# Kernel optimization log

Hardware: AMD Instinct MI355X
Metric: run time of the kernel (lower is better)

Reference implementation:

```python
import jax, jax.numpy as jnp
import numpy as np


def setup_inputs() -> dict:
    key = jax.random.key(0)
    B, D = 8192, 4096
    ks = jax.random.split(key, 6)
    s = 1.0 / np.sqrt(D)  # nn.init.uniform_(-1/sqrt(D), 1/sqrt(D))
    return {
        "u": jax.random.normal(ks[0], (B, D), dtype=jnp.float32),
        "w1": jax.random.uniform(ks[1], (D,), jnp.float32, -s, s),
        "w2": jax.random.uniform(ks[2], (D,), jnp.float32, -s, s),
        "w3": jax.random.uniform(ks[3], (D,), jnp.float32, -s, s),
        "bias1": jnp.ones((1,), jnp.float32),
        "bias2": jnp.ones((1,), jnp.float32),
        # nn.Linear(D, 1): kaiming-uniform-ish init approximated with same bound
        "delta_w": jax.random.uniform(ks[4], (1, D), jnp.float32, -s, s),
        "delta_b": jax.random.uniform(ks[5], (1,), jnp.float32, -s, s),
    }


def reference(u, w1, w2, w3, bias1, bias2, delta_w, delta_b):
    # select = softplus(delta(u) + bias1), shape [B]
    select = jax.nn.softplus(u @ delta_w.T + delta_b + bias1)[:, 0]
    # einsum('bi,b->b', M, x) == (sum_i M[b,i]) * x[b], so the recurrence
    # collapses to scalar-per-batch coefficients:
    a = select * (u @ w1)   # sum_i Abar[b,i] = select[b] * sum_i w1[i]*u[b,i]
    b = u @ w2              # sum_i Bbar[b,i]
    c = u @ w3              # sum_i Cbar[b,i]
    Dc = bias2[0]
    ut = u.T                # [T, B], time-major for scan; T == input_dim
    x0 = b * ut[0]          # xi at step 0; y[:,0] = x0 (no C/D term in original)

    def step(x, ui):
        xn = a * x + b * ui
        return xn, c * xn + Dc * ui

    _, ys = jax.lax.scan(step, x0, ut[1:])  # ys: [T-1, B]
    y = jnp.concatenate([x0[None, :], ys], axis=0).T  # [B, T]
    return y
```

## Files before the change

kernel.cpp:

```cpp
#include <hip/hip_runtime.h>
#include <math.h>


#define DDIM 4096
#define NCH  16

__device__ __forceinline__ float clf(float v) {
    int b   = __float_as_int(v);
    int mag = b & 0x7fffffff;
    if (mag >= 0x7F7A0000)
        v = __int_as_float((b & 0x80000000) | 0x7F7A0000);
    return v;
}

__device__ __forceinline__ float softplus_ref(float z) {
    return (z > 0.0f) ? (z + log1pf(expf(-z))) : log1pf(expf(z));
}

__global__ __launch_bounds__(256) void ssm_kernel(
    const float* __restrict__ u,
    const float* __restrict__ w1,
    const float* __restrict__ w2,
    const float* __restrict__ w3,
    const float* __restrict__ bias1,
    const float* __restrict__ bias2,
    const float* __restrict__ dw,
    const float* __restrict__ db,
    float* __restrict__ y)
{
    const int wid  = threadIdx.x >> 6;
    const int lane = threadIdx.x & 63;
    const int row  = (blockIdx.x << 2) + wid;

    const float* __restrict__ urow = u + (size_t)row * DDIM;
    float* __restrict__ yrow       = y + (size_t)row * DDIM;

    float4 uv[NCH];
    float s0 = 0.f, s1 = 0.f, s2 = 0.f, s3 = 0.f;
#pragma unroll
    for (int c = 0; c < NCH; ++c) {
        const int idx = c * 256 + lane * 4;
        uv[c] = *reinterpret_cast<const float4*>(urow + idx);
        const float4 dv = *reinterpret_cast<const float4*>(dw + idx);
        const float4 a1 = *reinterpret_cast<const float4*>(w1 + idx);
        const float4 a2 = *reinterpret_cast<const float4*>(w2 + idx);
        const float4 a3 = *reinterpret_cast<const float4*>(w3 + idx);
        s0 += uv[c].x * dv.x + uv[c].y * dv.y + uv[c].z * dv.z + uv[c].w * dv.w;
        s1 += uv[c].x * a1.x + uv[c].y * a1.y + uv[c].z * a1.z + uv[c].w * a1.w;
        s2 += uv[c].x * a2.x + uv[c].y * a2.y + uv[c].z * a2.z + uv[c].w * a2.w;
        s3 += uv[c].x * a3.x + uv[c].y * a3.y + uv[c].z * a3.z + uv[c].w * a3.w;
    }
#pragma unroll
    for (int d = 1; d < 64; d <<= 1) {
        s0 += __shfl_xor(s0, d, 64);
        s1 += __shfl_xor(s1, d, 64);
        s2 += __shfl_xor(s2, d, 64);
        s3 += __shfl_xor(s3, d, 64);
    }

    const float sel = softplus_ref(s0 + db[0] + bias1[0]);
    const float a   = clf(sel * s1);
    const float bb  = s2;
    const float cc  = s3;
    const float Dc  = bias2[0];

    const float a2p  = clf(a * a);
    const float r1   = clf(a2p * a2p);
    const float r2   = clf(r1 * r1);
    const float r4   = clf(r2 * r2);
    const float r8   = clf(r4 * r4);
    const float r16  = clf(r8 * r8);
    const float r32  = clf(r16 * r16);
    const float a256 = clf(r32 * r32);
    float P = 1.0f;
    if (lane & 1)  P = clf(P * r1);
    if (lane & 2)  P = clf(P * r2);
    if (lane & 4)  P = clf(P * r4);
    if (lane & 8)  P = clf(P * r8);
    if (lane & 16) P = clf(P * r16);
    if (lane & 32) P = clf(P * r32);

    float Bv[NCH];
#pragma unroll
    for (int c = 0; c < NCH; ++c) {
        float B = bb * uv[c].x;
        B = fmaf(a, B, bb * uv[c].y);
        B = fmaf(a, B, bb * uv[c].z);
        B = fmaf(a, B, bb * uv[c].w);
        Bv[c] = clf(B);
    }

#pragma unroll
    for (int c = 0; c < NCH; ++c) {
        float B = Bv[c];
        float t;
        t = __shfl_up(B, 1,  64); if (lane >= 1)  B = clf(fmaf(r1,  t, B));
        t = __shfl_up(B, 2,  64); if (lane >= 2)  B = clf(fmaf(r2,  t, B));
        t = __shfl_up(B, 4,  64); if (lane >= 4)  B = clf(fmaf(r4,  t, B));
        t = __shfl_up(B, 8,  64); if (lane >= 8)  B = clf(fmaf(r8,  t, B));
        t = __shfl_up(B, 16, 64); if (lane >= 16) B = clf(fmaf(r16, t, B));
        t = __shfl_up(B, 32, 64); if (lane >= 32) B = clf(fmaf(r32, t, B));
        Bv[c] = B;
    }

    float cr = 0.0f;
#pragma unroll
    for (int c = 0; c < NCH; ++c) {
        const int idx = c * 256 + lane * 4;
        const float T = __shfl(Bv[c], 63, 64);
        float Cprev   = __shfl_up(Bv[c], 1, 64);
        if (lane == 0) Cprev = 0.0f;

        const float xs = clf(fmaf(P, cr, Cprev));
        const float x0 = clf(fmaf(a, xs, bb * uv[c].x));
        const float x1 = clf(fmaf(a, x0, bb * uv[c].y));
        const float x2 = clf(fmaf(a, x1, bb * uv[c].z));
        const float x3 = clf(fmaf(a, x2, bb * uv[c].w));

        float4 yv;
        yv.x = clf(fmaf(cc, x0, Dc * uv[c].x));
        yv.y = clf(fmaf(cc, x1, Dc * uv[c].y));
        yv.z = clf(fmaf(cc, x2, Dc * uv[c].z));
        yv.w = clf(fmaf(cc, x3, Dc * uv[c].w));
        if (c == 0 && lane == 0) yv.x = x0;
        *reinterpret_cast<float4*>(yrow + idx) = yv;

        cr = clf(fmaf(a256, cr, T));
    }
}

extern "C" void kernel_launch(void* const* d_in, const int* in_sizes, int n_in,
                              void* d_out, int out_size, void* d_ws, size_t ws_size,
                              hipStream_t stream) {
    const float* u     = (const float*)d_in[0];
    const float* w1    = (const float*)d_in[1];
    const float* w2    = (const float*)d_in[2];
    const float* w3    = (const float*)d_in[3];
    const float* bias1 = (const float*)d_in[4];
    const float* bias2 = (const float*)d_in[5];
    const float* dw    = (const float*)d_in[6];
    const float* db    = (const float*)d_in[7];
    float* y = (float*)d_out;

    const int B = in_sizes[0] / DDIM;
    dim3 grid(B / 4), block(256);
    hipLaunchKernelGGL(ssm_kernel, grid, block, 0, stream,
                       u, w1, w2, w3, bias1, bias2, dw, db, y);
}
```

Measured before the change: 251.3 us.

## Split each row across four waves with LDS reduction and cross-wave scan carry

Each 256-thread block now handles one row instead of four, with each wave covering a quarter of the row. Dot-product partials are combined through shared memory, and the carry between waves is built from per-wave totals using a1024 powers. This cuts the registers each thread holds (4 float4 instead of 16), which should allow higher occupancy via launch_bounds(256,8) and better latency hiding. The cost is two block barriers and a small serial carry loop per wave.

```diff
diff --git a/kernel.cpp b/kernel.cpp
--- a/kernel.cpp
+++ b/kernel.cpp
@@ -3,7 +3,6 @@
 
 
 #define DDIM 4096
-#define NCH  16
 
 __device__ __forceinline__ float clf(float v) {
     int b   = __float_as_int(v);
@@ -17,7 +16,7 @@
     return (z > 0.0f) ? (z + log1pf(expf(-z))) : log1pf(expf(z));
 }
 
-__global__ __launch_bounds__(256) void ssm_kernel(
+__global__ __launch_bounds__(256, 8) void ssm_kernel(
     const float* __restrict__ u,
     const float* __restrict__ w1,
     const float* __restrict__ w2,
@@ -28,27 +27,31 @@
     const float* __restrict__ db,
     float* __restrict__ y)
 {
-    const int wid  = threadIdx.x >> 6;
-    const int lane = threadIdx.x & 63;
-    const int row  = (blockIdx.x << 2) + wid;
+    const int tid  = threadIdx.x;
+    const int wid  = tid >> 6;
+    const int lane = tid & 63;
+    const int row  = blockIdx.x;
 
     const float* __restrict__ urow = u + (size_t)row * DDIM;
     float* __restrict__ yrow       = y + (size_t)row * DDIM;
 
-    float4 uv[NCH];
+    __shared__ float4 red[4];
+    __shared__ float  wt[4];
+
+    float4 uv[4];
     float s0 = 0.f, s1 = 0.f, s2 = 0.f, s3 = 0.f;
 #pragma unroll
-    for (int c = 0; c < NCH; ++c) {
-        const int idx = c * 256 + lane * 4;
-        uv[c] = *reinterpret_cast<const float4*>(urow + idx);
+    for (int j = 0; j < 4; ++j) {
+        const int idx = (wid * 4 + j) * 256 + lane * 4;
+        uv[j] = *reinterpret_cast<const float4*>(urow + idx);
         const float4 dv = *reinterpret_cast<const float4*>(dw + idx);
         const float4 a1 = *reinterpret_cast<const float4*>(w1 + idx);
         const float4 a2 = *reinterpret_cast<const float4*>(w2 + idx);
         const float4 a3 = *reinterpret_cast<const float4*>(w3 + idx);
-        s0 += uv[c].x * dv.x + uv[c].y * dv.y + uv[c].z * dv.z + uv[c].w * dv.w;
-        s1 += uv[c].x * a1.x + uv[c].y * a1.y + uv[c].z * a1.z + uv[c].w * a1.w;
-        s2 += uv[c].x * a2.x + uv[c].y * a2.y + uv[c].z * a2.z + uv[c].w * a2.w;
-        s3 += uv[c].x * a3.x + uv[c].y * a3.y + uv[c].z * a3.z + uv[c].w * a3.w;
+        s0 += uv[j].x * dv.x + uv[j].y * dv.y + uv[j].z * dv.z + uv[j].w * dv.w;
+        s1 += uv[j].x * a1.x + uv[j].y * a1.y + uv[j].z * a1.z + uv[j].w * a1.w;
+        s2 += uv[j].x * a2.x + uv[j].y * a2.y + uv[j].z * a2.z + uv[j].w * a2.w;
+        s3 += uv[j].x * a3.x + uv[j].y * a3.y + uv[j].z * a3.z + uv[j].w * a3.w;
     }
 #pragma unroll
     for (int d = 1; d < 64; d <<= 1) {
@@ -57,6 +60,15 @@
         s2 += __shfl_xor(s2, d, 64);
         s3 += __shfl_xor(s3, d, 64);
     }
+    if (lane == 0) red[wid] = make_float4(s0, s1, s2, s3);
+    __syncthreads();
+    {
+        const float4 p0 = red[0], p1 = red[1], p2 = red[2], p3 = red[3];
+        s0 = p0.x + p1.x + p2.x + p3.x;
+        s1 = p0.y + p1.y + p2.y + p3.y;
+        s2 = p0.z + p1.z + p2.z + p3.z;
+        s3 = p0.w + p1.w + p2.w + p3.w;
+    }
 
     const float sel = softplus_ref(s0 + db[0] + bias1[0]);
     const float a   = clf(sel * s1);
@@ -64,14 +76,15 @@
     const float cc  = s3;
     const float Dc  = bias2[0];
 
-    const float a2p  = clf(a * a);
-    const float r1   = clf(a2p * a2p);
-    const float r2   = clf(r1 * r1);
-    const float r4   = clf(r2 * r2);
-    const float r8   = clf(r4 * r4);
-    const float r16  = clf(r8 * r8);
-    const float r32  = clf(r16 * r16);
-    const float a256 = clf(r32 * r32);
+    const float a2p   = clf(a * a);
+    const float r1    = clf(a2p * a2p);
+    const float r2    = clf(r1 * r1);
+    const float r4    = clf(r2 * r2);
+    const float r8    = clf(r4 * r4);
+    const float r16   = clf(r8 * r8);
+    const float r32   = clf(r16 * r16);
+    const float a256  = clf(r32 * r32);
+    const float a1024 = clf(clf(a256 * a256) * clf(a256 * a256));
     float P = 1.0f;
     if (lane & 1)  P = clf(P * r1);
     if (lane & 2)  P = clf(P * r2);
@@ -80,19 +93,19 @@
     if (lane & 16) P = clf(P * r16);
     if (lane & 32) P = clf(P * r32);
 
-    float Bv[NCH];
+    float Bv[4];
 #pragma unroll
-    for (int c = 0; c < NCH; ++c) {
-        float B = bb * uv[c].x;
-        B = fmaf(a, B, bb * uv[c].y);
-        B = fmaf(a, B, bb * uv[c].z);
-        B = fmaf(a, B, bb * uv[c].w);
-        Bv[c] = clf(B);
+    for (int j = 0; j < 4; ++j) {
+        float B = bb * uv[j].x;
+        B = fmaf(a, B, bb * uv[j].y);
+        B = fmaf(a, B, bb * uv[j].z);
+        B = fmaf(a, B, bb * uv[j].w);
+        Bv[j] = clf(B);
     }
 
 #pragma unroll
-    for (int c = 0; c < NCH; ++c) {
-        float B = Bv[c];
+    for (int j = 0; j < 4; ++j) {
+        float B = Bv[j];
         float t;
         t = __shfl_up(B, 1,  64); if (lane >= 1)  B = clf(fmaf(r1,  t, B));
         t = __shfl_up(B, 2,  64); if (lane >= 2)  B = clf(fmaf(r2,  t, B));
@@ -100,32 +113,44 @@
         t = __shfl_up(B, 8,  64); if (lane >= 8)  B = clf(fmaf(r8,  t, B));
         t = __shfl_up(B, 16, 64); if (lane >= 16) B = clf(fmaf(r16, t, B));
         t = __shfl_up(B, 32, 64); if (lane >= 32) B = clf(fmaf(r32, t, B));
-        Bv[c] = B;
+        Bv[j] = B;
     }
 
+    float T[4];
+#pragma unroll
+    for (int j = 0; j < 4; ++j) T[j] = __shfl(Bv[j], 63, 64);
+
+    float W = T[0];
+    W = clf(fmaf(a256, W, T[1]));
+    W = clf(fmaf(a256, W, T[2]));
+    W = clf(fmaf(a256, W, T[3]));
+    if (lane == 0) wt[wid] = W;
+    __syncthreads();
+
     float cr = 0.0f;
+    for (int w = 0; w < wid; ++w) cr = clf(fmaf(a1024, cr, wt[w]));
+
 #pragma unroll
-    for (int c = 0; c < NCH; ++c) {
-        const int idx = c * 256 + lane * 4;
-        const float T = __shfl(Bv[c], 63, 64);
-        float Cprev   = __shfl_up(Bv[c], 1, 64);
+    for (int j = 0; j < 4; ++j) {
+        const int idx = (wid * 4 + j) * 256 + lane * 4;
+        float Cprev = __shfl_up(Bv[j], 1, 64);
         if (lane == 0) Cprev = 0.0f;
 
         const float xs = clf(fmaf(P, cr, Cprev));
-        const float x0 = clf(fmaf(a, xs, bb * uv[c].x));
-        const float x1 = clf(fmaf(a, x0, bb * uv[c].y));
-        const float x2 = clf(fmaf(a, x1, bb * uv[c].z));
-        const float x3 = clf(fmaf(a, x2, bb * uv[c].w));
+        const float x0 = clf(fmaf(a, xs, bb * uv[j].x));
+        const float x1 = clf(fmaf(a, x0, bb * uv[j].y));
+        const float x2 = clf(fmaf(a, x1, bb * uv[j].z));
+        const float x3 = clf(fmaf(a, x2, bb * uv[j].w));
 
         float4 yv;
-        yv.x = clf(fmaf(cc, x0, Dc * uv[c].x));
-        yv.y = clf(fmaf(cc, x1, Dc * uv[c].y));
-        yv.z = clf(fmaf(cc, x2, Dc * uv[c].z));
-        yv.w = clf(fmaf(cc, x3, Dc * uv[c].w));
-        if (c == 0 && lane == 0) yv.x = x0;
+        yv.x = clf(fmaf(cc, x0, Dc * uv[j].x));
+        yv.y = clf(fmaf(cc, x1, Dc * uv[j].y));
+        yv.z = clf(fmaf(cc, x2, Dc * uv[j].z));
+        yv.w = clf(fmaf(cc, x3, Dc * uv[j].w));
+        if (j == 0 && tid == 0) yv.x = x0;
         *reinterpret_cast<float4*>(yrow + idx) = yv;
 
-        cr = clf(fmaf(a256, cr, T));
+        cr = clf(fmaf(a256, cr, T[j]));
     }
 }
 
@@ -143,7 +168,7 @@
     float* y = (float*)d_out;
 
     const int B = in_sizes[0] / DDIM;
-    dim3 grid(B / 4), block(256);
+    dim3 grid(B), block(256);
     hipLaunchKernelGGL(ssm_kernel, grid, block, 0, stream,
                        u, w1, w2, w3, bias1, bias2, dw, db, y);
 }
```

New measurement: 262.0 us. 4.3% more time.
